# Performance work log

Measured on AMD Instinct MI355X. Metric: run time of the kernel, lower is better.

Reference implementation:

```python
import jax, jax.numpy as jnp
import numpy as np

N = 100000   # nodes
E = 1600000  # edges (avg degree 16)
D = 128      # hidden_dim


def setup_inputs() -> dict:
    key = jax.random.key(0)
    k1, k2, k3, k4, k5, k6 = jax.random.split(key, 6)
    return {
        "t": jnp.zeros((), dtype=jnp.float32),  # unused by the ODE func
        "x": jax.random.normal(k1, (N, D), dtype=jnp.float32),
        "x0": jax.random.normal(k2, (N, D), dtype=jnp.float32),
        "alpha_train": jax.random.normal(k3, (N,), dtype=jnp.float32),
        "adj_values": jax.random.uniform(k4, (E,), dtype=jnp.float32),
        "adj_row": jax.random.randint(k5, (E,), 0, N, dtype=jnp.int32),
        "adj_col": jax.random.randint(k6, (E,), 0, N, dtype=jnp.int32),
    }


def reference(t, x, x0, alpha_train, adj_values, adj_row, adj_col):
    # alph = sigmoid(alpha_train).unsqueeze(1)  -> [N, 1]
    alph = jax.nn.sigmoid(alpha_train)[:, None]
    # ax = spmm(adj, x): COO gather of source-node features, scale by edge
    # value, scatter-add into destination rows. [N, D]
    ax = jax.ops.segment_sum(adj_values[:, None] * x[adj_col], adj_row,
                             num_segments=x.shape[0])
    # f = alph * 0.5 * (ax - x) + x0
    return alph * 0.5 * (ax - x) + x0
```

## Files before the change

### kernel.cpp

```cpp
#include <hip/hip_runtime.h>


#define DIM 128
#define RPB 128
#define ACHUNK 4096
#define BCAP 4096
#define NBMAX 1024

__device__ __forceinline__ float sigmoidf_(float a) {
    return 1.0f / (1.0f + __expf(-a));
}
__device__ __forceinline__ unsigned f2bf(float f) {
    unsigned u = __float_as_uint(f);
    return (u + 0x7FFFu + ((u >> 16) & 1u)) >> 16;
}

__global__ __launch_bounds__(256)
void xcast_kernel(const float* __restrict__ x, unsigned short* __restrict__ xb,
                  int n4) {
    int i = blockIdx.x * blockDim.x + threadIdx.x;
    if (i >= n4) return;
    float4 v = reinterpret_cast<const float4*>(x)[i];
    uint2 o;
    o.x = f2bf(v.x) | (f2bf(v.y) << 16);
    o.y = f2bf(v.z) | (f2bf(v.w) << 16);
    reinterpret_cast<uint2*>(xb)[i] = o;
}

__global__ __launch_bounds__(256)
void bucket_hist_kernel(const int* __restrict__ row, int* __restrict__ bhist,
                        int n_edges, int nb) {
    __shared__ int h[NBMAX];
    int t = threadIdx.x;
    for (int i = t; i < nb; i += 256) h[i] = 0;
    __syncthreads();
    int n4 = n_edges >> 2;
    for (int i = blockIdx.x * blockDim.x + t; i < n4;
         i += gridDim.x * blockDim.x) {
        int4 r = reinterpret_cast<const int4*>(row)[i];
        atomicAdd(&h[r.x >> 7], 1);
        atomicAdd(&h[r.y >> 7], 1);
        atomicAdd(&h[r.z >> 7], 1);
        atomicAdd(&h[r.w >> 7], 1);
    }
    if (blockIdx.x == 0 && t == 0) {
        for (int i = n4 << 2; i < n_edges; ++i)
            atomicAdd(&bhist[row[i] >> 7], 1);
    }
    __syncthreads();
    for (int i = t; i < nb; i += 256)
        if (h[i]) atomicAdd(&bhist[i], h[i]);
}

__global__ __launch_bounds__(1024)
void bucket_scan_kernel(const int* __restrict__ bhist, int* __restrict__ boffs,
                        int* __restrict__ bcur, int nb) {
    __shared__ int ts[1024];
    int t = threadIdx.x;
    ts[t] = (t < nb) ? bhist[t] : 0;
    __syncthreads();
    for (int off = 1; off < 1024; off <<= 1) {
        int u = (t >= off) ? ts[t - off] : 0;
        __syncthreads();
        ts[t] += u;
        __syncthreads();
    }
    if (t < nb) {
        int e = (t == 0) ? 0 : ts[t - 1];
        boffs[t] = e;
        bcur[t] = e;
    }
    if (t == nb - 1) boffs[nb] = ts[t];
}

__global__ __launch_bounds__(256)
void bin_kernel(const int* __restrict__ row, const int* __restrict__ col,
                const float* __restrict__ vals, int* __restrict__ bcursor,
                int2* __restrict__ epackA, int n_edges, int nb) {
    __shared__ int hist[NBMAX];
    __shared__ int lbase[NBMAX];
    __shared__ int gbase[NBMAX];
    __shared__ int lcur[NBMAX];
    __shared__ int ts[256];
    __shared__ int2 stage[ACHUNK];
    __shared__ int gpos[ACHUNK];
    int t = threadIdx.x;
    int base = blockIdx.x * ACHUNK;
    int m = n_edges - base;
    if (m > ACHUNK) m = ACHUNK;
    for (int i = t; i < nb; i += 256) hist[i] = 0;
    __syncthreads();
    for (int i = t; i < m; i += 256)
        atomicAdd(&hist[row[base + i] >> 7], 1);
    __syncthreads();
    int tb = t * 4;
    int h0 = (tb + 0 < nb) ? hist[tb + 0] : 0;
    int h1 = (tb + 1 < nb) ? hist[tb + 1] : 0;
    int h2 = (tb + 2 < nb) ? hist[tb + 2] : 0;
    int h3 = (tb + 3 < nb) ? hist[tb + 3] : 0;
    int s0 = h0, s1 = s0 + h1, s2 = s1 + h2, s3 = s2 + h3;
    ts[t] = s3;
    __syncthreads();
    for (int off = 1; off < 256; off <<= 1) {
        int u = (t >= off) ? ts[t - off] : 0;
        __syncthreads();
        ts[t] += u;
        __syncthreads();
    }
    int ex = (t == 0) ? 0 : ts[t - 1];
    if (tb + 0 < nb) lbase[tb + 0] = ex;
    if (tb + 1 < nb) lbase[tb + 1] = ex + s0;
    if (tb + 2 < nb) lbase[tb + 2] = ex + s1;
    if (tb + 3 < nb) lbase[tb + 3] = ex + s2;
    __syncthreads();
    for (int i = t; i < nb; i += 256) {
        gbase[i] = atomicAdd(&bcursor[i], hist[i]);
        lcur[i] = 0;
    }
    __syncthreads();
    for (int i = t; i < m; i += 256) {
        int r = row[base + i];
        int c = col[base + i];
        float v = vals[base + i];
        int bk = r >> 7;
        int lp = atomicAdd(&lcur[bk], 1);
        int sp = lbase[bk] + lp;
        stage[sp] = make_int2(((r & (RPB - 1)) << 17) | c, __float_as_int(v));
        gpos[sp] = gbase[bk] + lp;
    }
    __syncthreads();
    for (int i = t; i < m; i += 256)
        epackA[gpos[i]] = stage[i];
}

template <int USE_BF16>
__global__ __launch_bounds__(512)
void fused_sort_gather_kernel(const unsigned short* __restrict__ xb,
                              const float* __restrict__ x,
                              const float* __restrict__ x0,
                              const float* __restrict__ alpha,
                              const int* __restrict__ boffs,
                              const int2* __restrict__ epackA,
                              float* __restrict__ out, int n_nodes) {
    __shared__ int2 eout[BCAP];
    __shared__ int rowstart[RPB];
    __shared__ int rowcur[RPB];
    __shared__ float sval[RPB];
    int b = blockIdx.x, t = threadIdx.x;
    int r0 = b * RPB;
    int begin = boffs[b], end = boffs[b + 1];
    int n = end - begin;
    if (t < RPB) {
        int r = r0 + t;
        sval[t] = (r < n_nodes) ? 0.5f * sigmoidf_(alpha[r]) : 0.f;
        rowstart[t] = 0;
    }
    __syncthreads();
    int wave = t >> 6, lane = t & 63;
    const unsigned* xbp = reinterpret_cast<const unsigned*>(xb);
    const float2* xp = reinterpret_cast<const float2*>(x);
    if (n <= BCAP) {
        for (int i = t; i < n; i += 512)
            atomicAdd(&rowstart[epackA[begin + i].x >> 17], 1);
        __syncthreads();
        if (t < RPB) rowcur[t] = rowstart[t];
        __syncthreads();
        for (int off = 1; off < RPB; off <<= 1) {
            int u = (t < RPB && t >= off) ? rowcur[t - off] : 0;
            __syncthreads();
            if (t < RPB) rowcur[t] += u;
            __syncthreads();
        }
        if (t < RPB) {
            int excl = rowcur[t] - rowstart[t];
            rowstart[t] = excl;
            rowcur[t] = excl;
        }
        __syncthreads();
        for (int i = t; i < n; i += 512) {
            int2 e = epackA[begin + i];
            int pos = atomicAdd(&rowcur[e.x >> 17], 1);
            eout[pos] = make_int2(e.x & 0x1FFFF, e.y);
        }
        __syncthreads();
        for (int q = 0; q < 16; ++q) {
            int lr = wave * 16 + q;
            int r = r0 + lr;
            if (r >= n_nodes) break;
            float s = sval[lr];
            int rb = r * 64;
            float2 xv = xp[rb + lane];
            float2 acc = reinterpret_cast<const float2*>(x0)[rb + lane];
            acc.x -= s * xv.x;
            acc.y -= s * xv.y;
            int k = rowstart[lr];
            int stop = (lr + 1 < RPB) ? rowstart[lr + 1] : n;
            for (; k + 8 <= stop; k += 8) {
                float w[8];
                if (USE_BF16) {
                    unsigned d[8];
#pragma unroll
                    for (int j = 0; j < 8; ++j) {
                        int2 e = eout[k + j];
                        w[j] = s * __int_as_float(e.y);
                        d[j] = xbp[(size_t)e.x * 64 + lane];
                    }
#pragma unroll
                    for (int j = 0; j < 8; ++j) {
                        acc.x += w[j] * __uint_as_float((d[j] & 0xFFFFu) << 16);
                        acc.y += w[j] * __uint_as_float(d[j] & 0xFFFF0000u);
                    }
                } else {
                    float2 v[8];
#pragma unroll
                    for (int j = 0; j < 8; ++j) {
                        int2 e = eout[k + j];
                        w[j] = s * __int_as_float(e.y);
                        v[j] = xp[(size_t)e.x * 64 + lane];
                    }
#pragma unroll
                    for (int j = 0; j < 8; ++j) {
                        acc.x += w[j] * v[j].x;
                        acc.y += w[j] * v[j].y;
                    }
                }
            }
            for (; k < stop; ++k) {
                int2 e = eout[k];
                float w = s * __int_as_float(e.y);
                if (USE_BF16) {
                    unsigned d = xbp[(size_t)e.x * 64 + lane];
                    acc.x += w * __uint_as_float((d & 0xFFFFu) << 16);
                    acc.y += w * __uint_as_float(d & 0xFFFF0000u);
                } else {
                    float2 v = xp[(size_t)e.x * 64 + lane];
                    acc.x += w * v.x;
                    acc.y += w * v.y;
                }
            }
            reinterpret_cast<float2*>(out)[rb + lane] = acc;
        }
    } else {
        for (int q = 0; q < 16; ++q) {
            int lr = wave * 16 + q;
            int r = r0 + lr;
            if (r >= n_nodes) break;
            float s = sval[lr];
            int rb = r * 64;
            float2 xv = xp[rb + lane];
            float2 acc = reinterpret_cast<const float2*>(x0)[rb + lane];
            acc.x -= s * xv.x;
            acc.y -= s * xv.y;
            for (int i = 0; i < n; ++i) {
                int2 e = epackA[begin + i];
                if ((e.x >> 17) == lr) {
                    float w = s * __int_as_float(e.y);
                    if (USE_BF16) {
                        unsigned d = xbp[(size_t)(e.x & 0x1FFFF) * 64 + lane];
                        acc.x += w * __uint_as_float((d & 0xFFFFu) << 16);
                        acc.y += w * __uint_as_float(d & 0xFFFF0000u);
                    } else {
                        float2 v = xp[(size_t)(e.x & 0x1FFFF) * 64 + lane];
                        acc.x += w * v.x;
                        acc.y += w * v.y;
                    }
                }
            }
            reinterpret_cast<float2*>(out)[rb + lane] = acc;
        }
    }
}

extern "C" void kernel_launch(void* const* d_in, const int* in_sizes, int n_in,
                              void* d_out, int out_size, void* d_ws, size_t ws_size,
                              hipStream_t stream) {
    const float* x     = (const float*)d_in[1];
    const float* x0    = (const float*)d_in[2];
    const float* alpha = (const float*)d_in[3];
    const float* vals  = (const float*)d_in[4];
    const int*   row   = (const int*)d_in[5];
    const int*   col   = (const int*)d_in[6];
    float* out = (float*)d_out;

    int n_nodes = in_sizes[3];
    int n_edges = in_sizes[4];
    int nb = (n_nodes + RPB - 1) / RPB;

    size_t xb_bytes = (size_t)n_nodes * DIM * sizeof(unsigned short);
    size_t ep_bytes = (size_t)((n_edges + 3) & ~3) * sizeof(int2);
    size_t meta_bytes = (size_t)(NBMAX + NBMAX + 16 + NBMAX) * sizeof(int);
    int use_bf16 = (ws_size >= xb_bytes + ep_bytes + meta_bytes + 512) ? 1 : 0;

    unsigned short* xxb;
    int2* epackA;
    int* bhist;
    if (use_bf16) {
        xxb    = (unsigned short*)d_ws;
        epackA = (int2*)((char*)d_ws + xb_bytes);
        bhist  = (int*)((char*)epackA + ep_bytes);
    } else {
        xxb    = nullptr;
        epackA = (int2*)d_ws;
        bhist  = (int*)((char*)epackA + ep_bytes);
    }
    int* boffs = bhist + NBMAX;
    int* bcur  = boffs + NBMAX + 16;

    hipMemsetAsync(bhist, 0, NBMAX * sizeof(int), stream);

    if (use_bf16) {
        int n4 = (n_nodes * DIM) >> 2;
        xcast_kernel<<<(n4 + 255) / 256, 256, 0, stream>>>(x, xxb, n4);
    }
    bucket_hist_kernel<<<256, 256, 0, stream>>>(row, bhist, n_edges, nb);
    bucket_scan_kernel<<<1, 1024, 0, stream>>>(bhist, boffs, bcur, nb);
    {
        int grid = (n_edges + ACHUNK - 1) / ACHUNK;
        bin_kernel<<<grid, 256, 0, stream>>>(row, col, vals, bcur, epackA,
                                             n_edges, nb);
    }
    if (use_bf16) {
        fused_sort_gather_kernel<1><<<nb, 512, 0, stream>>>(
            xxb, x, x0, alpha, boffs, epackA, out, n_nodes);
    } else {
        fused_sort_gather_kernel<0><<<nb, 512, 0, stream>>>(
            xxb, x, x0, alpha, boffs, epackA, out, n_nodes);
    }
}
```

Measured before the change: 139.4 us.

## Halve rows per bucket, fuse bf16 cast with histogram, trim bin-kernel staging

Buckets shrink from 128 to 64 rows, so there are twice as many gather blocks, each with a smaller shared-memory edge buffer, and the scan handles two buckets per thread. The bf16 cast and bucket histogram kernels merge into one launch. The bin kernel stores a 16-bit bucket id instead of a full global position per edge, cutting shared memory use. The self term now reads the bf16 copy of x instead of fp32. This lowers launch count and shared-memory pressure, but a 64-row bucket overflows BCAP more easily and then falls back to the slow unsorted path.

```diff
diff --git a/kernel.cpp b/kernel.cpp
--- a/kernel.cpp
+++ b/kernel.cpp
@@ -2,10 +2,12 @@
 
 
 #define DIM 128
-#define RPB 128
+#define RPB 64
+#define RSHIFT 6
 #define ACHUNK 4096
-#define BCAP 4096
-#define NBMAX 1024
+#define BCAP 2048
+#define NBMAX 2048
+#define HISTB 128
 
 __device__ __forceinline__ float sigmoidf_(float a) {
     return 1.0f / (1.0f + __expf(-a));
@@ -16,39 +18,39 @@
 }
 
 __global__ __launch_bounds__(256)
-void xcast_kernel(const float* __restrict__ x, unsigned short* __restrict__ xb,
-                  int n4) {
-    int i = blockIdx.x * blockDim.x + threadIdx.x;
-    if (i >= n4) return;
-    float4 v = reinterpret_cast<const float4*>(x)[i];
-    uint2 o;
-    o.x = f2bf(v.x) | (f2bf(v.y) << 16);
-    o.y = f2bf(v.z) | (f2bf(v.w) << 16);
-    reinterpret_cast<uint2*>(xb)[i] = o;
-}
-
-__global__ __launch_bounds__(256)
-void bucket_hist_kernel(const int* __restrict__ row, int* __restrict__ bhist,
-                        int n_edges, int nb) {
+void xcast_hist_kernel(const float* __restrict__ x,
+                       unsigned short* __restrict__ xb, int n4,
+                       const int* __restrict__ row, int* __restrict__ bhist,
+                       int n_edges, int nb, int xg) {
     __shared__ int h[NBMAX];
+    if ((int)blockIdx.x < xg) {
+        int i = blockIdx.x * 256 + threadIdx.x;
+        if (i >= n4) return;
+        float4 v = reinterpret_cast<const float4*>(x)[i];
+        uint2 o;
+        o.x = f2bf(v.x) | (f2bf(v.y) << 16);
+        o.y = f2bf(v.z) | (f2bf(v.w) << 16);
+        reinterpret_cast<uint2*>(xb)[i] = o;
+        return;
+    }
     int t = threadIdx.x;
-    for (int i = t; i < nb; i += 256) h[i] = 0;
-    __syncthreads();
-    int n4 = n_edges >> 2;
-    for (int i = blockIdx.x * blockDim.x + t; i < n4;
-         i += gridDim.x * blockDim.x) {
+    int bid = blockIdx.x - xg;
+    for (int i = t; i < NBMAX; i += 256) h[i] = 0;
+    __syncthreads();
+    int e4 = n_edges >> 2;
+    for (int i = bid * 256 + t; i < e4; i += HISTB * 256) {
         int4 r = reinterpret_cast<const int4*>(row)[i];
-        atomicAdd(&h[r.x >> 7], 1);
-        atomicAdd(&h[r.y >> 7], 1);
-        atomicAdd(&h[r.z >> 7], 1);
-        atomicAdd(&h[r.w >> 7], 1);
-    }
-    if (blockIdx.x == 0 && t == 0) {
-        for (int i = n4 << 2; i < n_edges; ++i)
-            atomicAdd(&bhist[row[i] >> 7], 1);
-    }
-    __syncthreads();
-    for (int i = t; i < nb; i += 256)
+        atomicAdd(&h[r.x >> RSHIFT], 1);
+        atomicAdd(&h[r.y >> RSHIFT], 1);
+        atomicAdd(&h[r.z >> RSHIFT], 1);
+        atomicAdd(&h[r.w >> RSHIFT], 1);
+    }
+    if (bid == 0 && t == 0) {
+        for (int i = e4 << 2; i < n_edges; ++i)
+            atomicAdd(&bhist[row[i] >> RSHIFT], 1);
+    }
+    __syncthreads();
+    for (int i = t; i < NBMAX; i += 256)
         if (h[i]) atomicAdd(&bhist[i], h[i]);
 }
 
@@ -57,7 +59,10 @@
                         int* __restrict__ bcur, int nb) {
     __shared__ int ts[1024];
     int t = threadIdx.x;
-    ts[t] = (t < nb) ? bhist[t] : 0;
+    int i0 = 2 * t, i1 = 2 * t + 1;
+    int v0 = (i0 < nb) ? bhist[i0] : 0;
+    int v1 = (i1 < nb) ? bhist[i1] : 0;
+    ts[t] = v0 + v1;
     __syncthreads();
     for (int off = 1; off < 1024; off <<= 1) {
         int u = (t >= off) ? ts[t - off] : 0;
@@ -65,12 +70,10 @@
         ts[t] += u;
         __syncthreads();
     }
-    if (t < nb) {
-        int e = (t == 0) ? 0 : ts[t - 1];
-        boffs[t] = e;
-        bcur[t] = e;
-    }
-    if (t == nb - 1) boffs[nb] = ts[t];
+    int ex = (t == 0) ? 0 : ts[t - 1];
+    if (i0 < nb) { boffs[i0] = ex;      bcur[i0] = ex; }
+    if (i1 < nb) { boffs[i1] = ex + v0; bcur[i1] = ex + v0; }
+    if (t == 1023) boffs[nb] = ts[1023];
 }
 
 __global__ __launch_bounds__(256)
@@ -83,23 +86,22 @@
     __shared__ int lcur[NBMAX];
     __shared__ int ts[256];
     __shared__ int2 stage[ACHUNK];
-    __shared__ int gpos[ACHUNK];
+    __shared__ unsigned short bkid[ACHUNK];
     int t = threadIdx.x;
     int base = blockIdx.x * ACHUNK;
     int m = n_edges - base;
     if (m > ACHUNK) m = ACHUNK;
-    for (int i = t; i < nb; i += 256) hist[i] = 0;
+    for (int i = t; i < NBMAX; i += 256) hist[i] = 0;
     __syncthreads();
     for (int i = t; i < m; i += 256)
-        atomicAdd(&hist[row[base + i] >> 7], 1);
-    __syncthreads();
-    int tb = t * 4;
-    int h0 = (tb + 0 < nb) ? hist[tb + 0] : 0;
-    int h1 = (tb + 1 < nb) ? hist[tb + 1] : 0;
-    int h2 = (tb + 2 < nb) ? hist[tb + 2] : 0;
-    int h3 = (tb + 3 < nb) ? hist[tb + 3] : 0;
-    int s0 = h0, s1 = s0 + h1, s2 = s1 + h2, s3 = s2 + h3;
-    ts[t] = s3;
+        atomicAdd(&hist[row[base + i] >> RSHIFT], 1);
+    __syncthreads();
+    int tb = t * 8;
+    int hh[8];
+    int run = 0;
+#pragma unroll
+    for (int j = 0; j < 8; ++j) { hh[j] = hist[tb + j]; run += hh[j]; }
+    ts[t] = run;
     __syncthreads();
     for (int off = 1; off < 256; off <<= 1) {
         int u = (t >= off) ? ts[t - off] : 0;
@@ -108,10 +110,8 @@
         __syncthreads();
     }
     int ex = (t == 0) ? 0 : ts[t - 1];
-    if (tb + 0 < nb) lbase[tb + 0] = ex;
-    if (tb + 1 < nb) lbase[tb + 1] = ex + s0;
-    if (tb + 2 < nb) lbase[tb + 2] = ex + s1;
-    if (tb + 3 < nb) lbase[tb + 3] = ex + s2;
+#pragma unroll
+    for (int j = 0; j < 8; ++j) { lbase[tb + j] = ex; ex += hh[j]; }
     __syncthreads();
     for (int i = t; i < nb; i += 256) {
         gbase[i] = atomicAdd(&bcursor[i], hist[i]);
@@ -122,15 +122,17 @@
         int r = row[base + i];
         int c = col[base + i];
         float v = vals[base + i];
-        int bk = r >> 7;
+        int bk = r >> RSHIFT;
         int lp = atomicAdd(&lcur[bk], 1);
         int sp = lbase[bk] + lp;
         stage[sp] = make_int2(((r & (RPB - 1)) << 17) | c, __float_as_int(v));
-        gpos[sp] = gbase[bk] + lp;
-    }
-    __syncthreads();
-    for (int i = t; i < m; i += 256)
-        epackA[gpos[i]] = stage[i];
+        bkid[sp] = (unsigned short)bk;
+    }
+    __syncthreads();
+    for (int i = t; i < m; i += 256) {
+        int bk = bkid[i];
+        epackA[gbase[bk] + (i - lbase[bk])] = stage[i];
+    }
 }
 
 template <int USE_BF16>
@@ -183,16 +185,22 @@
             eout[pos] = make_int2(e.x & 0x1FFFF, e.y);
         }
         __syncthreads();
-        for (int q = 0; q < 16; ++q) {
-            int lr = wave * 16 + q;
+        for (int q = 0; q < 8; ++q) {
+            int lr = wave * 8 + q;
             int r = r0 + lr;
             if (r >= n_nodes) break;
             float s = sval[lr];
             int rb = r * 64;
-            float2 xv = xp[rb + lane];
             float2 acc = reinterpret_cast<const float2*>(x0)[rb + lane];
-            acc.x -= s * xv.x;
-            acc.y -= s * xv.y;
+            if (USE_BF16) {
+                unsigned dx = xbp[rb + lane];
+                acc.x -= s * __uint_as_float((dx & 0xFFFFu) << 16);
+                acc.y -= s * __uint_as_float(dx & 0xFFFF0000u);
+            } else {
+                float2 xv = xp[rb + lane];
+                acc.x -= s * xv.x;
+                acc.y -= s * xv.y;
+            }
             int k = rowstart[lr];
             int stop = (lr + 1 < RPB) ? rowstart[lr + 1] : n;
             for (; k + 8 <= stop; k += 8) {
@@ -241,16 +249,22 @@
             reinterpret_cast<float2*>(out)[rb + lane] = acc;
         }
     } else {
-        for (int q = 0; q < 16; ++q) {
-            int lr = wave * 16 + q;
+        for (int q = 0; q < 8; ++q) {
+            int lr = wave * 8 + q;
             int r = r0 + lr;
             if (r >= n_nodes) break;
             float s = sval[lr];
             int rb = r * 64;
-            float2 xv = xp[rb + lane];
             float2 acc = reinterpret_cast<const float2*>(x0)[rb + lane];
-            acc.x -= s * xv.x;
-            acc.y -= s * xv.y;
+            if (USE_BF16) {
+                unsigned dx = xbp[rb + lane];
+                acc.x -= s * __uint_as_float((dx & 0xFFFFu) << 16);
+                acc.y -= s * __uint_as_float(dx & 0xFFFF0000u);
+            } else {
+                float2 xv = xp[rb + lane];
+                acc.x -= s * xv.x;
+                acc.y -= s * xv.y;
+            }
             for (int i = 0; i < n; ++i) {
                 int2 e = epackA[begin + i];
                 if ((e.x >> 17) == lr) {
@@ -308,11 +322,12 @@
 
     hipMemsetAsync(bhist, 0, NBMAX * sizeof(int), stream);
 
-    if (use_bf16) {
-        int n4 = (n_nodes * DIM) >> 2;
-        xcast_kernel<<<(n4 + 255) / 256, 256, 0, stream>>>(x, xxb, n4);
-    }
-    bucket_hist_kernel<<<256, 256, 0, stream>>>(row, bhist, n_edges, nb);
+    {
+        int n4 = use_bf16 ? ((n_nodes * DIM) >> 2) : 0;
+        int xg = use_bf16 ? ((n4 + 255) / 256) : 0;
+        xcast_hist_kernel<<<xg + HISTB, 256, 0, stream>>>(
+            x, xxb, n4, row, bhist, n_edges, nb, xg);
+    }
     bucket_scan_kernel<<<1, 1024, 0, stream>>>(bhist, boffs, bcur, nb);
     {
         int grid = (n_edges + ACHUNK - 1) / ACHUNK;
```

New measurement: 134.6 us. 3.5% less time.
